# Optimization experiments

Hardware: AMD Instinct MI355X
Metric: run time of the kernel (lower is better)

## Reference

```python
import jax, jax.numpy as jnp
import numpy as np

B, C_IN, L = 4, 512, 16384
C_RED = C_IN // 2  # q/k/v reduced channels = 256
BL = 64            # sliding-window block size
NEG = -jnp.inf


def setup_inputs() -> dict:
    key = jax.random.key(0)
    ks = jax.random.split(key, 8)
    x1 = jax.random.normal(ks[0], (B, C_IN, L), dtype=jnp.float32)
    x2 = jax.random.normal(ks[1], (B, C_IN, L), dtype=jnp.float32)
    mask = jnp.ones((B, 1, L), dtype=jnp.float32)
    s = 0.02
    Wq = jax.random.normal(ks[2], (C_RED, C_IN), dtype=jnp.float32) * s
    Wk = jax.random.normal(ks[3], (C_RED, C_IN), dtype=jnp.float32) * s
    Wv = jax.random.normal(ks[4], (C_RED, C_IN), dtype=jnp.float32) * s
    Wo = jax.random.normal(ks[5], (C_IN, C_RED), dtype=jnp.float32) * s
    bq = jnp.zeros((C_RED,), jnp.float32)
    bk = jnp.zeros((C_RED,), jnp.float32)
    bv = jnp.zeros((C_RED,), jnp.float32)
    bo = jnp.zeros((C_IN,), jnp.float32)
    return {"x1": x1, "x2": x2, "mask": mask, "Wq": Wq, "bq": bq,
            "Wk": Wk, "bk": bk, "Wv": Wv, "bv": bv, "Wo": Wo, "bo": bo}


def _conv1x1(W, b, x):
    # x: (B, Cin, L) -> (B, Cout, L)
    return jnp.einsum('oc,bcl->bol', W, x) + b[None, :, None]


def reference(x1, x2, mask, Wq, bq, Wk, bk, Wv, bv, Wo, bo):
    # encoder stage: value comes from x1 (x2 unused)
    q = _conv1x1(Wq, bq, x1)  # (B, C, L)
    k = _conv1x1(Wk, bk, x1)
    v = _conv1x1(Wv, bv, x1)

    Bq, C, Lq = q.shape
    bl = BL
    nb = (Lq + bl - 1) // bl
    pad = nb * bl - Lq
    if pad > 0:
        q = jnp.pad(q, ((0, 0), (0, 0), (0, pad)))
        k = jnp.pad(k, ((0, 0), (0, 0), (0, pad)))
        v = jnp.pad(v, ((0, 0), (0, 0), (0, pad)))
        mask = jnp.pad(mask, ((0, 0), (0, 0), (0, pad)))

    # non-overlapping windows: (B, C, nb, bl)
    qb = q.reshape(Bq, C, nb, bl)
    kb = k.reshape(Bq, C, nb, bl)
    vb = v.reshape(Bq, C, nb, bl)
    mb = mask.reshape(Bq, 1, nb, bl)  # (B,1,nb,bl)

    scale = 1.0 / jnp.sqrt(jnp.float32(C))
    # per-block attention scores: (B, nb, bl_i, bl_j)
    scores = jnp.einsum('bcni,bcnj->bnij', qb, kb) * scale
    key_mask = mb[:, 0, :, None, :]  # (B, nb, 1, bl_j)
    scores = jnp.where(key_mask == 0, NEG, scores)
    probs = jax.nn.softmax(scores, axis=-1)
    attn = jnp.einsum('bnij,bcnj->bcni', probs, vb)  # (B, C, nb, bl)

    h = jax.nn.relu(attn)
    out = jnp.einsum('oc,bcni->boni', Wo, h) + bo[None, :, None, None]
    out = out.reshape(Bq, Wo.shape[0], nb * bl)
    if pad > 0:
        out = out[:, :, :Lq]
    return out
```

## Files before the change

### kernel.cpp

```cpp
#include <hip/hip_runtime.h>
#include <hip/hip_fp16.h>
#include <stdint.h>

#define BB    4
#define CIN   512
#define CRED  256
#define LL    16384
#define NBLK  256
#define WELEM 131072

typedef _Float16 half8 __attribute__((ext_vector_type(8)));
typedef float    f32x4 __attribute__((ext_vector_type(4)));

#define SWZ(r) (((r)&7)<<4)

#define QBASE   524288
#define MAT_E   16777216
#define WS_NEED ((size_t)(QBASE + 3 * MAT_E) * 2)

__global__ void convert_weights(const float* __restrict__ Wq,
                                const float* __restrict__ Wk,
                                const float* __restrict__ Wv,
                                const float* __restrict__ Wo,
                                _Float16* __restrict__ dst) {
    int i = blockIdx.x * blockDim.x + threadIdx.x;
    int m = i >> 17;
    int e = i & (WELEM - 1);
    const float* src = (m == 0) ? Wq : (m == 1) ? Wk : (m == 2) ? Wv : Wo;
    dst[(size_t)m * WELEM + e] = (_Float16)src[e];
}

__global__ __launch_bounds__(256, 2)
void qkv_gemm(const float* __restrict__ x1, const _Float16* __restrict__ W,
              const float* __restrict__ bq, const float* __restrict__ bk,
              const float* __restrict__ bv, _Float16* __restrict__ ws) {
    extern __shared__ char lds[];
    const int tid = threadIdx.x;
    const int wid = tid >> 6;
    const int l15 = tid & 15;
    const int l4  = (tid & 63) >> 4;
    const int b   = blockIdx.x >> 8;
    const int n   = blockIdx.x & 255;

    {
        const int jx = tid & 15;
        const int rg = tid >> 4;
        const float* xp = x1 + ((size_t)b * CIN + 8 * rg) * LL + n * 64 + 4 * jx;
        f32x4 st[4][8];
        #pragma unroll
        for (int i = 0; i < 4; ++i)
            #pragma unroll
            for (int r8 = 0; r8 < 8; ++r8)
                st[i][r8] = *(const f32x4*)(xp + (size_t)(128 * i + r8) * LL);
        asm volatile("" ::: "memory");
        #pragma unroll
        for (int i = 0; i < 4; ++i) {
            #pragma unroll
            for (int u = 0; u < 4; ++u) {
                const int j = 4 * jx + u;
                union { _Float16 h[8]; half8 v; } pk;
                #pragma unroll
                for (int r8 = 0; r8 < 8; ++r8) pk.h[r8] = (_Float16)st[i][r8][u];
                *(half8*)(lds + j * 1024 + ((16 * rg + 256 * i) ^ SWZ(j))) = pk.v;
            }
        }
    }
    __syncthreads();

    #pragma unroll
    for (int p = 0; p < 3; ++p) {
        f32x4 acc[4][4];
        #pragma unroll
        for (int mt = 0; mt < 4; ++mt)
            #pragma unroll
            for (int q = 0; q < 4; ++q) acc[mt][q] = (f32x4){0.f, 0.f, 0.f, 0.f};

        const _Float16* wp = W + (size_t)p * WELEM
                           + (size_t)(wid * 64 + l15) * CIN + l4 * 8;

        half8 wf[2][4], xf[2][4];
        #pragma unroll
        for (int mt = 0; mt < 4; ++mt) wf[0][mt] = *(const half8*)(wp + mt * 16 * CIN);
        #pragma unroll
        for (int nt = 0; nt < 4; ++nt) {
            const int j = nt * 16 + l15;
            xf[0][nt] = *(const half8*)(lds + j * 1024 + ((l4 * 16) ^ SWZ(j)));
        }

        #pragma unroll
        for (int ks = 0; ks < 16; ++ks) {
            const int c = ks & 1, nx = c ^ 1;
            if (ks < 15) {
                const int kb = (ks + 1) * 64 + l4 * 16;
                #pragma unroll
                for (int mt = 0; mt < 4; ++mt)
                    wf[nx][mt] = *(const half8*)(wp + mt * 16 * CIN + (ks + 1) * 32);
                #pragma unroll
                for (int nt = 0; nt < 4; ++nt) {
                    const int j = nt * 16 + l15;
                    xf[nx][nt] = *(const half8*)(lds + j * 1024 + (kb ^ SWZ(j)));
                }
            }
            #pragma unroll
            for (int mt = 0; mt < 4; ++mt)
                #pragma unroll
                for (int nt = 0; nt < 4; ++nt)
                    acc[mt][nt] = __builtin_amdgcn_mfma_f32_16x16x32_f16(
                        wf[c][mt], xf[c][nt], acc[mt][nt], 0, 0, 0);
        }

        if (p < 2) {
            _Float16* dst = ws + QBASE + (size_t)p * MAT_E
                          + ((size_t)b * LL + n * 64) * CRED;
            const float* bias = p ? bk : bq;
            #pragma unroll
            for (int mt = 0; mt < 4; ++mt) {
                const int c0 = wid * 64 + mt * 16 + l4 * 4;
                f32x4 b4 = *(const f32x4*)(bias + c0);
                #pragma unroll
                for (int nt = 0; nt < 4; ++nt) {
                    const int pos = nt * 16 + l15;
                    union { _Float16 h[4]; uint64_t q; } pk;
                    #pragma unroll
                    for (int ri = 0; ri < 4; ++ri)
                        pk.h[ri] = (_Float16)(acc[mt][nt][ri] + b4[ri]);
                    *(uint64_t*)(dst + (size_t)pos * CRED + c0) = pk.q;
                }
            }
        } else {
            _Float16* vdst = ws + QBASE + 2 * (size_t)MAT_E
                           + (size_t)b * CRED * LL + n * 64;
            #pragma unroll
            for (int mt = 0; mt < 4; ++mt) {
                const int c0 = wid * 64 + mt * 16 + l4 * 4;
                f32x4 b4 = *(const f32x4*)(bv + c0);
                #pragma unroll
                for (int nt = 0; nt < 4; ++nt) {
                    const int pos = nt * 16 + l15;
                    #pragma unroll
                    for (int ri = 0; ri < 4; ++ri)
                        vdst[(size_t)(c0 + ri) * LL + pos] =
                            (_Float16)(acc[mt][nt][ri] + b4[ri]);
                }
            }
        }
    }
}

#define BH_OFF 0
#define BP_OFF 32768
#define LDS_B  40960

__global__ __launch_bounds__(256, 3)
void attn_out(const float* __restrict__ mask, const _Float16* __restrict__ ws,
              const float* __restrict__ bo, float* __restrict__ out) {
    extern __shared__ char lds[];
    const int tid = threadIdx.x;
    const int wid = tid >> 6;
    const int l15 = tid & 15;
    const int l4  = (tid & 63) >> 4;
    const int b   = blockIdx.x >> 8;
    const int n   = blockIdx.x & 255;

    const _Float16* qt = ws + QBASE + ((size_t)b * LL + n * 64) * CRED;
    const _Float16* kt = qt + MAT_E;
    const _Float16* vt = ws + QBASE + 2 * (size_t)MAT_E + (size_t)b * CRED * LL + n * 64;
    const _Float16* Wo = ws + 3 * (size_t)WELEM;

    {
        const int i0 = wid * 16;
        f32x4 sa[4];
        #pragma unroll
        for (int jt = 0; jt < 4; ++jt) sa[jt] = (f32x4){0.f, 0.f, 0.f, 0.f};
        #pragma unroll
        for (int ks = 0; ks < 8; ++ks) {
            half8 qa = *(const half8*)(qt + (size_t)(i0 + l15) * CRED + ks * 32 + l4 * 8);
            #pragma unroll
            for (int jt = 0; jt < 4; ++jt) {
                half8 kf = *(const half8*)(kt + (size_t)(jt * 16 + l15) * CRED + ks * 32 + l4 * 8);
                sa[jt] = __builtin_amdgcn_mfma_f32_16x16x32_f16(qa, kf, sa[jt], 0, 0, 0);
            }
        }
        float msk[4];
        #pragma unroll
        for (int jt = 0; jt < 4; ++jt)
            msk[jt] = mask[(size_t)b * LL + n * 64 + jt * 16 + l15];
        #pragma unroll
        for (int ri = 0; ri < 4; ++ri) {
            float v[4];
            #pragma unroll
            for (int jt = 0; jt < 4; ++jt)
                v[jt] = (msk[jt] == 0.f) ? -1e30f : sa[jt][ri] * 0.0625f;
            float mx = fmaxf(fmaxf(v[0], v[1]), fmaxf(v[2], v[3]));
            mx = fmaxf(mx, __shfl_xor(mx, 1));
            mx = fmaxf(mx, __shfl_xor(mx, 2));
            mx = fmaxf(mx, __shfl_xor(mx, 4));
            mx = fmaxf(mx, __shfl_xor(mx, 8));
            float e[4], sum = 0.f;
            #pragma unroll
            for (int jt = 0; jt < 4; ++jt) { e[jt] = __expf(v[jt] - mx); sum += e[jt]; }
            sum += __shfl_xor(sum, 1);
            sum += __shfl_xor(sum, 2);
            sum += __shfl_xor(sum, 4);
            sum += __shfl_xor(sum, 8);
            const float inv = 1.f / sum;
            const int i = i0 + l4 * 4 + ri;
            #pragma unroll
            for (int jt = 0; jt < 4; ++jt) {
                const int j = jt * 16 + l15;
                *(_Float16*)(lds + BP_OFF + i * 128 + ((2 * j) ^ SWZ(i))) =
                    (_Float16)(e[jt] * inv);
            }
        }
    }
    __syncthreads();

    {
        const int cb = wid * 64;
        f32x4 pv[4][4];
        #pragma unroll
        for (int m = 0; m < 4; ++m)
            #pragma unroll
            for (int q = 0; q < 4; ++q) pv[m][q] = (f32x4){0.f, 0.f, 0.f, 0.f};
        #pragma unroll
        for (int ks = 0; ks < 2; ++ks) {
            const int kb = ks * 64 + l4 * 16;
            half8 pb[4];
            #pragma unroll
            for (int nt = 0; nt < 4; ++nt) {
                const int i = nt * 16 + l15;
                pb[nt] = *(const half8*)(lds + BP_OFF + i * 128 + (kb ^ SWZ(i)));
            }
            #pragma unroll
            for (int mt = 0; mt < 4; ++mt) {
                half8 va = *(const half8*)(vt + (size_t)(cb + mt * 16 + l15) * LL + ks * 32 + l4 * 8);
                #pragma unroll
                for (int nt = 0; nt < 4; ++nt)
                    pv[mt][nt] = __builtin_amdgcn_mfma_f32_16x16x32_f16(va, pb[nt], pv[mt][nt], 0, 0, 0);
            }
        }
        #pragma unroll
        for (int mt = 0; mt < 4; ++mt) {
            const int c0 = cb + mt * 16 + l4 * 4;
            #pragma unroll
            for (int nt = 0; nt < 4; ++nt) {
                const int j = nt * 16 + l15;
                union { _Float16 h[4]; uint64_t q; } hp;
                #pragma unroll
                for (int ri = 0; ri < 4; ++ri)
                    hp.h[ri] = (_Float16)fmaxf(pv[mt][nt][ri], 0.f);
                *(uint64_t*)(lds + BH_OFF + j * 512 + ((2 * c0) ^ SWZ(j))) = hp.q;
            }
        }
    }
    __syncthreads();

    #pragma unroll
    for (int op = 0; op < 2; ++op) {
        const int mbo = wid * 128 + op * 64;
        const _Float16* wob = Wo + (size_t)(mbo + l15) * CRED + l4 * 8;
        f32x4 oa[4][4];
        #pragma unroll
        for (int m = 0; m < 4; ++m)
            #pragma unroll
            for (int q = 0; q < 4; ++q) oa[m][q] = (f32x4){0.f, 0.f, 0.f, 0.f};
        #pragma unroll 4
        for (int ks = 0; ks < 8; ++ks) {
            const int kb = ks * 64 + l4 * 16;
            half8 hb[4];
            #pragma unroll
            for (int nt = 0; nt < 4; ++nt) {
                const int i = nt * 16 + l15;
                hb[nt] = *(const half8*)(lds + BH_OFF + i * 512 + (kb ^ SWZ(i)));
            }
            #pragma unroll
            for (int mt = 0; mt < 4; ++mt) {
                half8 wa = *(const half8*)(wob + mt * 16 * CRED + ks * 32);
                #pragma unroll
                for (int nt = 0; nt < 4; ++nt)
                    oa[mt][nt] = __builtin_amdgcn_mfma_f32_16x16x32_f16(wa, hb[nt], oa[mt][nt], 0, 0, 0);
            }
        }
        #pragma unroll
        for (int mt = 0; mt < 4; ++mt) {
            const int o0 = mbo + mt * 16 + l4 * 4;
            f32x4 bov = *(const f32x4*)(bo + o0);
            #pragma unroll
            for (int ri = 0; ri < 4; ++ri) {
                float* orow = out + ((size_t)b * CIN + (o0 + ri)) * LL + n * 64;
                #pragma unroll
                for (int nt = 0; nt < 4; ++nt)
                    orow[nt * 16 + l15] = oa[mt][nt][ri] + bov[ri];
            }
        }
    }
}

#define XT_OFF 0
#define Q_OFF  0
#define K_OFF  32768
#define V_OFF  32768
#define H_OFF  0
#define P_OFF  65536
#define MSK_OFF 73728
#define LDS_BYTES 73984

__global__ __launch_bounds__(256, 2)
void att_fused(const float* __restrict__ x1, const float* __restrict__ mask,
               const _Float16* __restrict__ W,
               const float* __restrict__ bq, const float* __restrict__ bk,
               const float* __restrict__ bv, const float* __restrict__ bo,
               float* __restrict__ out) {
    extern __shared__ char lds[];
    const int tid  = threadIdx.x;
    const int wid  = tid >> 6;
    const int lane = tid & 63;
    const int l15  = lane & 15;
    const int l4   = lane >> 4;
    const int blk  = blockIdx.x;
    const int b    = blk >> 8;
    const int n    = blk & 255;

    const _Float16* Wq = W;
    const _Float16* Wk = W + WELEM;
    const _Float16* Wv = W + 2 * WELEM;
    const _Float16* Wo = W + 3 * WELEM;

    {
        const int jx = tid & 15;
        const int rb = tid >> 4;
        const float* xbase = x1 + ((size_t)b * CIN + 2 * rb) * LL + n * 64 + 4 * jx;
        #pragma unroll
        for (int i = 0; i < 16; ++i) {
            f32x4 a = *(const f32x4*)(xbase + (size_t)(32 * i) * LL);
            f32x4 c = *(const f32x4*)(xbase + (size_t)(32 * i + 1) * LL);
            const int col = 4 * rb + 64 * i;
            #pragma unroll
            for (int u = 0; u < 4; ++u) {
                union { _Float16 h[2]; uint32_t w; } p;
                p.h[0] = (_Float16)a[u];
                p.h[1] = (_Float16)c[u];
                const int j = 4 * jx + u;
                *(uint32_t*)(lds + XT_OFF + j * 1024 + (col ^ SWZ(j))) = p.w;
            }
        }
        if (tid < 64)
            *(float*)(lds + MSK_OFF + tid * 4) = mask[(size_t)b * LL + n * 64 + tid];
    }
    __syncthreads();

    uint64_t qh[4][4], kh[4][4], vh[4][4];
    #pragma unroll
    for (int pass = 0; pass < 4; ++pass) {
        f32x4 aQ[4], aK[4], aV[4];
        #pragma unroll
        for (int q = 0; q < 4; ++q) {
            aQ[q] = (f32x4){0.f, 0.f, 0.f, 0.f};
            aK[q] = (f32x4){0.f, 0.f, 0.f, 0.f};
            aV[q] = (f32x4){0.f, 0.f, 0.f, 0.f};
        }
// ... 138 lines not shown
            }
            #pragma unroll
            for (int mt = 0; mt < 4; ++mt) {
                const int c = cb + mt * 16 + l15;
                half8 va = *(const half8*)(lds + V_OFF + c * 128 + (kb ^ SWZ(c)));
                #pragma unroll
                for (int nt = 0; nt < 4; ++nt)
                    pv[mt][nt] = __builtin_amdgcn_mfma_f32_16x16x32_f16(va, pb[nt], pv[mt][nt], 0, 0, 0);
            }
        }
        #pragma unroll
        for (int mt = 0; mt < 4; ++mt) {
            const int c0 = cb + mt * 16 + l4 * 4;
            #pragma unroll
            for (int nt = 0; nt < 4; ++nt) {
                const int j = nt * 16 + l15;
                union { _Float16 h[4]; uint64_t q; } hp;
                #pragma unroll
                for (int ri = 0; ri < 4; ++ri)
                    hp.h[ri] = (_Float16)fmaxf(pv[mt][nt][ri], 0.f);
                *(uint64_t*)(lds + H_OFF + j * 512 + ((2 * c0) ^ SWZ(j))) = hp.q;
            }
        }
    }
    __syncthreads();

    #pragma unroll
    for (int op = 0; op < 2; ++op) {
        const int mbo = wid * 128 + op * 64;
        const _Float16* wob = Wo + (size_t)(mbo + l15) * CRED + l4 * 8;
        f32x4 oa[4][4];
        #pragma unroll
        for (int m = 0; m < 4; ++m)
            #pragma unroll
            for (int q = 0; q < 4; ++q) oa[m][q] = (f32x4){0.f, 0.f, 0.f, 0.f};
        #pragma unroll 4
        for (int ks = 0; ks < 8; ++ks) {
            const int kb = ks * 64 + l4 * 16;
            half8 hb[4];
            #pragma unroll
            for (int nt = 0; nt < 4; ++nt) {
                const int i = nt * 16 + l15;
                hb[nt] = *(const half8*)(lds + H_OFF + i * 512 + (kb ^ SWZ(i)));
            }
            #pragma unroll
            for (int mt = 0; mt < 4; ++mt) {
                half8 wa = *(const half8*)(wob + mt * 16 * CRED + ks * 32);
                #pragma unroll
                for (int nt = 0; nt < 4; ++nt)
                    oa[mt][nt] = __builtin_amdgcn_mfma_f32_16x16x32_f16(wa, hb[nt], oa[mt][nt], 0, 0, 0);
            }
        }
        #pragma unroll
        for (int mt = 0; mt < 4; ++mt) {
            const int o0 = mbo + mt * 16 + l4 * 4;
            f32x4 bov = *(const f32x4*)(bo + o0);
            #pragma unroll
            for (int ri = 0; ri < 4; ++ri) {
                float* orow = out + ((size_t)b * CIN + (o0 + ri)) * LL + n * 64;
                #pragma unroll
                for (int nt = 0; nt < 4; ++nt)
                    orow[nt * 16 + l15] = oa[mt][nt][ri] + bov[ri];
            }
        }
    }
}

extern "C" void kernel_launch(void* const* d_in, const int* in_sizes, int n_in,
                              void* d_out, int out_size, void* d_ws, size_t ws_size,
                              hipStream_t stream) {
    const float* x1   = (const float*)d_in[0];
    const float* mask = (const float*)d_in[2];
    const float* Wq   = (const float*)d_in[3];
    const float* bq   = (const float*)d_in[4];
    const float* Wk   = (const float*)d_in[5];
    const float* bk   = (const float*)d_in[6];
    const float* Wv   = (const float*)d_in[7];
    const float* bv   = (const float*)d_in[8];
    const float* Wo   = (const float*)d_in[9];
    const float* bo   = (const float*)d_in[10];
    float* out = (float*)d_out;
    _Float16* wbuf = (_Float16*)d_ws;

    convert_weights<<<2048, 256, 0, stream>>>(Wq, Wk, Wv, Wo, wbuf);

    if (ws_size >= WS_NEED) {
        (void)hipFuncSetAttribute((const void*)qkv_gemm,
                                  hipFuncAttributeMaxDynamicSharedMemorySize, 65536);
        qkv_gemm<<<BB * NBLK, 256, 65536, stream>>>(x1, wbuf, bq, bk, bv, wbuf);
        attn_out<<<BB * NBLK, 256, LDS_B, stream>>>(mask, wbuf, bo, out);
    } else {
        (void)hipFuncSetAttribute((const void*)att_fused,
                                  hipFuncAttributeMaxDynamicSharedMemorySize, LDS_BYTES);
        att_fused<<<BB * NBLK, 256, LDS_BYTES, stream>>>(x1, mask, wbuf, bq, bk, bv, bo, out);
    }
}
```

Before: 199.0 us.

## Split x transpose into separate kernel and tile-local V layout in QKV GEMM

Adds an x_transpose kernel that converts x1 to fp16 and writes per-tile transposed blocks to workspace, so the QKV GEMM reads x fragments straight from global memory instead of staging them through 64KB of LDS. The GEMM now uses 512 threads with two m-tiles per wave. V is written into the x tile region it just consumed, stored contiguously as channel x 64 per tile rather than strided by L. This adds an extra kernel launch and a full fp16 round trip of x through memory, in exchange for higher occupancy and better-coalesced V stores and loads.

```diff
diff --git a/kernel.cpp b/kernel.cpp
--- a/kernel.cpp
+++ b/kernel.cpp
@@ -14,9 +14,12 @@
 
 #define SWZ(r) (((r)&7)<<4)
 
-#define QBASE   524288
-#define MAT_E   16777216
-#define WS_NEED ((size_t)(QBASE + 3 * MAT_E) * 2)
+#define XB      524288
+#define TILE_EL 32768
+#define XTV_EL  (1024 * TILE_EL)
+#define QB2     (XB + XTV_EL)
+#define KB2     (QB2 + 16777216)
+#define WS_NEED ((size_t)(KB2 + 16777216) * 2)
 
 __global__ void convert_weights(const float* __restrict__ Wq,
                                 const float* __restrict__ Wk,
@@ -30,79 +33,86 @@
     dst[(size_t)m * WELEM + e] = (_Float16)src[e];
 }
 
-__global__ __launch_bounds__(256, 2)
-void qkv_gemm(const float* __restrict__ x1, const _Float16* __restrict__ W,
-              const float* __restrict__ bq, const float* __restrict__ bk,
-              const float* __restrict__ bv, _Float16* __restrict__ ws) {
-    extern __shared__ char lds[];
+__global__ __launch_bounds__(256, 4)
+void x_transpose(const float* __restrict__ x1, _Float16* __restrict__ ws) {
+    __shared__ char lds[16384];
+    const int tid = threadIdx.x;
+    const int blk = blockIdx.x;
+    const int t   = blk >> 2;
+    const int cc  = blk & 3;
+    const int b   = t >> 8, n = t & 255;
+    const int jx  = tid & 15;
+    const int rg  = tid >> 4;
+
+    const float* xp = x1 + ((size_t)b * CIN + cc * 128 + 8 * rg) * LL + n * 64 + 4 * jx;
+    f32x4 r[8];
+    #pragma unroll
+    for (int k = 0; k < 8; ++k)
+        r[k] = *(const f32x4*)(xp + (size_t)k * LL);
+    asm volatile("" ::: "memory");
+    #pragma unroll
+    for (int u = 0; u < 4; ++u) {
+        const int j = 4 * jx + u;
+        union { _Float16 h[8]; half8 v; } pk;
+        #pragma unroll
+        for (int k = 0; k < 8; ++k) pk.h[k] = (_Float16)r[k][u];
+        *(half8*)(lds + j * 256 + ((16 * rg) ^ SWZ(j))) = pk.v;
+    }
+    __syncthreads();
+    _Float16* dst = ws + XB + (size_t)t * TILE_EL + cc * 8192;
+    const int l4d = tid >> 6, jd = tid & 63;
+    #pragma unroll
+    for (int rr = 0; rr < 4; ++rr) {
+        half8 v = *(const half8*)(lds + jd * 256 + ((rr * 64 + l4d * 16) ^ SWZ(jd)));
+        *(half8*)(dst + rr * 2048 + tid * 8) = v;
+    }
+}
+
+__global__ __launch_bounds__(512, 4)
+void qkv_gemm2(const _Float16* __restrict__ W,
+               const float* __restrict__ bq, const float* __restrict__ bk,
+               const float* __restrict__ bv, _Float16* ws) {
     const int tid = threadIdx.x;
     const int wid = tid >> 6;
     const int l15 = tid & 15;
     const int l4  = (tid & 63) >> 4;
-    const int b   = blockIdx.x >> 8;
-    const int n   = blockIdx.x & 255;
-
-    {
-        const int jx = tid & 15;
-        const int rg = tid >> 4;
-        const float* xp = x1 + ((size_t)b * CIN + 8 * rg) * LL + n * 64 + 4 * jx;
-        f32x4 st[4][8];
-        #pragma unroll
-        for (int i = 0; i < 4; ++i)
-            #pragma unroll
-            for (int r8 = 0; r8 < 8; ++r8)
-                st[i][r8] = *(const f32x4*)(xp + (size_t)(128 * i + r8) * LL);
-        asm volatile("" ::: "memory");
-        #pragma unroll
-        for (int i = 0; i < 4; ++i) {
-            #pragma unroll
-            for (int u = 0; u < 4; ++u) {
-                const int j = 4 * jx + u;
-                union { _Float16 h[8]; half8 v; } pk;
-                #pragma unroll
-                for (int r8 = 0; r8 < 8; ++r8) pk.h[r8] = (_Float16)st[i][r8][u];
-                *(half8*)(lds + j * 1024 + ((16 * rg + 256 * i) ^ SWZ(j))) = pk.v;
-            }
-        }
-    }
-    __syncthreads();
+    const int t   = blockIdx.x;
+    const int b   = t >> 8, n = t & 255;
+
+    const _Float16* xt = ws + XB + (size_t)t * TILE_EL;
+    f32x4 accV[2][4];
 
     #pragma unroll
     for (int p = 0; p < 3; ++p) {
-        f32x4 acc[4][4];
-        #pragma unroll
-        for (int mt = 0; mt < 4; ++mt)
+        f32x4 acc[2][4];
+        #pragma unroll
+        for (int mt = 0; mt < 2; ++mt)
             #pragma unroll
             for (int q = 0; q < 4; ++q) acc[mt][q] = (f32x4){0.f, 0.f, 0.f, 0.f};
 
         const _Float16* wp = W + (size_t)p * WELEM
-                           + (size_t)(wid * 64 + l15) * CIN + l4 * 8;
-
-        half8 wf[2][4], xf[2][4];
-        #pragma unroll
-        for (int mt = 0; mt < 4; ++mt) wf[0][mt] = *(const half8*)(wp + mt * 16 * CIN);
-        #pragma unroll
-        for (int nt = 0; nt < 4; ++nt) {
-            const int j = nt * 16 + l15;
-            xf[0][nt] = *(const half8*)(lds + j * 1024 + ((l4 * 16) ^ SWZ(j)));
-        }
+                           + (size_t)(wid * 32 + l15) * CIN + l4 * 8;
+        half8 wf[2][2], xf[2][4];
+        #pragma unroll
+        for (int mt = 0; mt < 2; ++mt) wf[0][mt] = *(const half8*)(wp + mt * 16 * CIN);
+        #pragma unroll
+        for (int nt = 0; nt < 4; ++nt)
+            xf[0][nt] = *(const half8*)(xt + l4 * 512 + (nt * 16 + l15) * 8);
 
         #pragma unroll
         for (int ks = 0; ks < 16; ++ks) {
             const int c = ks & 1, nx = c ^ 1;
             if (ks < 15) {
-                const int kb = (ks + 1) * 64 + l4 * 16;
-                #pragma unroll
-                for (int mt = 0; mt < 4; ++mt)
+                #pragma unroll
+                for (int mt = 0; mt < 2; ++mt)
                     wf[nx][mt] = *(const half8*)(wp + mt * 16 * CIN + (ks + 1) * 32);
                 #pragma unroll
-                for (int nt = 0; nt < 4; ++nt) {
-                    const int j = nt * 16 + l15;
-                    xf[nx][nt] = *(const half8*)(lds + j * 1024 + (kb ^ SWZ(j)));
-                }
-            }
-            #pragma unroll
-            for (int mt = 0; mt < 4; ++mt)
+                for (int nt = 0; nt < 4; ++nt)
+                    xf[nx][nt] = *(const half8*)(xt + (ks + 1) * 2048 + l4 * 512
+                                                 + (nt * 16 + l15) * 8);
+            }
+            #pragma unroll
+            for (int mt = 0; mt < 2; ++mt)
                 #pragma unroll
                 for (int nt = 0; nt < 4; ++nt)
                     acc[mt][nt] = __builtin_amdgcn_mfma_f32_16x16x32_f16(
@@ -110,12 +120,11 @@
         }
 
         if (p < 2) {
-            _Float16* dst = ws + QBASE + (size_t)p * MAT_E
-                          + ((size_t)b * LL + n * 64) * CRED;
+            _Float16* dst = ws + (p ? KB2 : QB2) + ((size_t)b * LL + n * 64) * CRED;
             const float* bias = p ? bk : bq;
             #pragma unroll
-            for (int mt = 0; mt < 4; ++mt) {
-                const int c0 = wid * 64 + mt * 16 + l4 * 4;
+            for (int mt = 0; mt < 2; ++mt) {
+                const int c0 = wid * 32 + mt * 16 + l4 * 4;
                 f32x4 b4 = *(const f32x4*)(bias + c0);
                 #pragma unroll
                 for (int nt = 0; nt < 4; ++nt) {
@@ -128,20 +137,27 @@
                 }
             }
         } else {
-            _Float16* vdst = ws + QBASE + 2 * (size_t)MAT_E
-                           + (size_t)b * CRED * LL + n * 64;
-            #pragma unroll
-            for (int mt = 0; mt < 4; ++mt) {
-                const int c0 = wid * 64 + mt * 16 + l4 * 4;
-                f32x4 b4 = *(const f32x4*)(bv + c0);
-                #pragma unroll
-                for (int nt = 0; nt < 4; ++nt) {
-                    const int pos = nt * 16 + l15;
-                    #pragma unroll
-                    for (int ri = 0; ri < 4; ++ri)
-                        vdst[(size_t)(c0 + ri) * LL + pos] =
-                            (_Float16)(acc[mt][nt][ri] + b4[ri]);
-                }
+            #pragma unroll
+            for (int mt = 0; mt < 2; ++mt)
+                #pragma unroll
+                for (int q = 0; q < 4; ++q) accV[mt][q] = acc[mt][q];
+        }
+    }
+
+    __syncthreads();
+    {
+        _Float16* vdst = ws + XB + (size_t)t * TILE_EL;
+        #pragma unroll
+        for (int mt = 0; mt < 2; ++mt) {
+            const int c0 = wid * 32 + mt * 16 + l4 * 4;
+            f32x4 b4 = *(const f32x4*)(bv + c0);
+            #pragma unroll
+            for (int nt = 0; nt < 4; ++nt) {
+                const int pos = nt * 16 + l15;
+                #pragma unroll
+                for (int ri = 0; ri < 4; ++ri)
+                    vdst[(size_t)(c0 + ri) * 64 + pos] =
+                        (_Float16)(accV[mt][nt][ri] + b4[ri]);
             }
         }
     }
@@ -161,10 +177,11 @@
     const int l4  = (tid & 63) >> 4;
     const int b   = blockIdx.x >> 8;
     const int n   = blockIdx.x & 255;
-
-    const _Float16* qt = ws + QBASE + ((size_t)b * LL + n * 64) * CRED;
-    const _Float16* kt = qt + MAT_E;
-    const _Float16* vt = ws + QBASE + 2 * (size_t)MAT_E + (size_t)b * CRED * LL + n * 64;
+    const int t   = blockIdx.x;
+
+    const _Float16* qt = ws + QB2 + ((size_t)b * LL + n * 64) * CRED;
+    const _Float16* kt = ws + KB2 + ((size_t)b * LL + n * 64) * CRED;
+    const _Float16* vt = ws + XB + (size_t)t * TILE_EL;
     const _Float16* Wo = ws + 3 * (size_t)WELEM;
 
     {
@@ -233,7 +250,7 @@
             }
             #pragma unroll
             for (int mt = 0; mt < 4; ++mt) {
-                half8 va = *(const half8*)(vt + (size_t)(cb + mt * 16 + l15) * LL + ks * 32 + l4 * 8);
+                half8 va = *(const half8*)(vt + (size_t)(cb + mt * 16 + l15) * 64 + ks * 32 + l4 * 8);
                 #pragma unroll
                 for (int nt = 0; nt < 4; ++nt)
                     pv[mt][nt] = __builtin_amdgcn_mfma_f32_16x16x32_f16(va, pb[nt], pv[mt][nt], 0, 0, 0);
@@ -583,9 +600,8 @@
     convert_weights<<<2048, 256, 0, stream>>>(Wq, Wk, Wv, Wo, wbuf);
 
     if (ws_size >= WS_NEED) {
-        (void)hipFuncSetAttribute((const void*)qkv_gemm,
-                                  hipFuncAttributeMaxDynamicSharedMemorySize, 65536);
-        qkv_gemm<<<BB * NBLK, 256, 65536, stream>>>(x1, wbuf, bq, bk, bv, wbuf);
+        x_transpose<<<4096, 256, 0, stream>>>(x1, wbuf);
+        qkv_gemm2<<<BB * NBLK, 512, 0, stream>>>(wbuf, bq, bk, bv, wbuf);
         attn_out<<<BB * NBLK, 256, LDS_B, stream>>>(mask, wbuf, bo, out);
     } else {
         (void)hipFuncSetAttribute((const void*)att_fused,
```

After: 261.2 us. 31.2% more time.

## Pre-swizzle weights into MFMA fragment layout and store V per-block contiguously

Applied to the files above, without the earlier changes.

Weights are converted into a fragment-major fp16 layout so each lane's half8 MFMA operand comes from a contiguous chunk, which makes weight loads coalesced. The QKV kernel now computes Q and K together in one pass over the LDS x tile, with staggered k-order per wave. V is staged through LDS and written as a contiguous per-block tile instead of strided rows of length L. The attention kernel reads V and Wo with the new layouts. The price is higher register pressure from the two live accumulator sets and the loss of the explicit double-buffered prefetch.

```diff
diff --git a/kernel.cpp b/kernel.cpp
--- a/kernel.cpp
+++ b/kernel.cpp
@@ -14,15 +14,38 @@
 
 #define SWZ(r) (((r)&7)<<4)
 
-#define QBASE   524288
-#define MAT_E   16777216
-#define WS_NEED ((size_t)(QBASE + 3 * MAT_E) * 2)
-
-__global__ void convert_weights(const float* __restrict__ Wq,
-                                const float* __restrict__ Wk,
-                                const float* __restrict__ Wv,
-                                const float* __restrict__ Wo,
-                                _Float16* __restrict__ dst) {
+#define QB      524288
+#define KB      (QB + 16777216)
+#define VB      (KB + 16777216)
+#define WS_NEED ((size_t)(VB + 16777216) * 2)
+
+__global__ void convert_weights_fm(const float* __restrict__ Wq,
+                                   const float* __restrict__ Wk,
+                                   const float* __restrict__ Wv,
+                                   const float* __restrict__ Wo,
+                                   _Float16* __restrict__ dst) {
+    int i = blockIdx.x * blockDim.x + threadIdx.x;
+    int p = i >> 17;
+    int e17 = i & (WELEM - 1);
+    const float* src = (p == 0) ? Wq : (p == 1) ? Wk : (p == 2) ? Wv : Wo;
+    const int Kd = (p < 3) ? 512 : 256;
+    const int sh = (p < 3) ? 13 : 12;
+    const int m16 = e17 >> sh;
+    const int rem = e17 & ((1 << sh) - 1);
+    const int ks  = rem >> 9;
+    const int l4  = (rem >> 7) & 3;
+    const int l15 = (rem >> 3) & 15;
+    const int ee  = rem & 7;
+    const int r = m16 * 16 + l15;
+    const int k = ks * 32 + l4 * 8 + ee;
+    dst[(size_t)p * WELEM + e17] = (_Float16)src[(size_t)r * Kd + k];
+}
+
+__global__ void convert_weights_rm(const float* __restrict__ Wq,
+                                   const float* __restrict__ Wk,
+                                   const float* __restrict__ Wv,
+                                   const float* __restrict__ Wo,
+                                   _Float16* __restrict__ dst) {
     int i = blockIdx.x * blockDim.x + threadIdx.x;
     int m = i >> 17;
     int e = i & (WELEM - 1);
@@ -31,16 +54,16 @@
 }
 
 __global__ __launch_bounds__(256, 2)
-void qkv_gemm(const float* __restrict__ x1, const _Float16* __restrict__ W,
-              const float* __restrict__ bq, const float* __restrict__ bk,
-              const float* __restrict__ bv, _Float16* __restrict__ ws) {
+void qkv_fused(const float* __restrict__ x1, const _Float16* __restrict__ W,
+               const float* __restrict__ bq, const float* __restrict__ bk,
+               const float* __restrict__ bv, _Float16* __restrict__ ws) {
     extern __shared__ char lds[];
     const int tid = threadIdx.x;
     const int wid = tid >> 6;
     const int l15 = tid & 15;
     const int l4  = (tid & 63) >> 4;
-    const int b   = blockIdx.x >> 8;
-    const int n   = blockIdx.x & 255;
+    const int t   = blockIdx.x;
+    const int b   = t >> 8, n = t & 255;
 
     {
         const int jx = tid & 15;
@@ -67,82 +90,113 @@
     }
     __syncthreads();
 
+    const int fbase = l4 * 128 + l15 * 8;
+
+    f32x4 aQ[4][4], aK[4][4];
     #pragma unroll
-    for (int p = 0; p < 3; ++p) {
-        f32x4 acc[4][4];
-        #pragma unroll
-        for (int mt = 0; mt < 4; ++mt)
-            #pragma unroll
-            for (int q = 0; q < 4; ++q) acc[mt][q] = (f32x4){0.f, 0.f, 0.f, 0.f};
-
-        const _Float16* wp = W + (size_t)p * WELEM
-                           + (size_t)(wid * 64 + l15) * CIN + l4 * 8;
-
-        half8 wf[2][4], xf[2][4];
-        #pragma unroll
-        for (int mt = 0; mt < 4; ++mt) wf[0][mt] = *(const half8*)(wp + mt * 16 * CIN);
-        #pragma unroll
-        for (int nt = 0; nt < 4; ++nt) {
-            const int j = nt * 16 + l15;
-            xf[0][nt] = *(const half8*)(lds + j * 1024 + ((l4 * 16) ^ SWZ(j)));
-        }
-
-        #pragma unroll
-        for (int ks = 0; ks < 16; ++ks) {
-            const int c = ks & 1, nx = c ^ 1;
-            if (ks < 15) {
-                const int kb = (ks + 1) * 64 + l4 * 16;
-                #pragma unroll
-                for (int mt = 0; mt < 4; ++mt)
-                    wf[nx][mt] = *(const half8*)(wp + mt * 16 * CIN + (ks + 1) * 32);
+    for (int mt = 0; mt < 4; ++mt)
+        #pragma unroll
+        for (int q = 0; q < 4; ++q) {
+            aQ[mt][q] = (f32x4){0.f, 0.f, 0.f, 0.f};
+            aK[mt][q] = (f32x4){0.f, 0.f, 0.f, 0.f};
+        }
+    {
+        const _Float16* wqf = W + (size_t)(wid * 4) * 8192 + fbase;
+        const _Float16* wkf = wqf + WELEM;
+        #pragma unroll
+        for (int i = 0; i < 16; ++i) {
+            const int ks = (i + wid * 4) & 15;
+            half8 xf[4];
+            #pragma unroll
+            for (int nt = 0; nt < 4; ++nt) {
+                const int j = nt * 16 + l15;
+                xf[nt] = *(const half8*)(lds + j * 1024 + ((ks * 64 + l4 * 16) ^ SWZ(j)));
+            }
+            #pragma unroll
+            for (int mt = 0; mt < 4; ++mt) {
+                half8 qf = *(const half8*)(wqf + mt * 8192 + ks * 512);
+                half8 kf = *(const half8*)(wkf + mt * 8192 + ks * 512);
                 #pragma unroll
                 for (int nt = 0; nt < 4; ++nt) {
-                    const int j = nt * 16 + l15;
-                    xf[nx][nt] = *(const half8*)(lds + j * 1024 + (kb ^ SWZ(j)));
+                    aQ[mt][nt] = __builtin_amdgcn_mfma_f32_16x16x32_f16(qf, xf[nt], aQ[mt][nt], 0, 0, 0);
+                    aK[mt][nt] = __builtin_amdgcn_mfma_f32_16x16x32_f16(kf, xf[nt], aK[mt][nt], 0, 0, 0);
                 }
             }
-            #pragma unroll
-            for (int mt = 0; mt < 4; ++mt)
+        }
+    }
+    {
+        _Float16* qdst = ws + QB + (size_t)t * 16384;
+        _Float16* kdst = ws + KB + (size_t)t * 16384;
+        #pragma unroll
+        for (int mt = 0; mt < 4; ++mt) {
+            const int c0 = wid * 64 + mt * 16 + l4 * 4;
+            f32x4 bq4 = *(const f32x4*)(bq + c0);
+            f32x4 bk4 = *(const f32x4*)(bk + c0);
+            #pragma unroll
+            for (int nt = 0; nt < 4; ++nt) {
+                const int pos = nt * 16 + l15;
+                union { _Float16 h[4]; uint64_t q; } qp, kp;
+                #pragma unroll
+                for (int ri = 0; ri < 4; ++ri) {
+                    qp.h[ri] = (_Float16)(aQ[mt][nt][ri] + bq4[ri]);
+                    kp.h[ri] = (_Float16)(aK[mt][nt][ri] + bk4[ri]);
+                }
+                *(uint64_t*)(qdst + (size_t)pos * 256 + c0) = qp.q;
+                *(uint64_t*)(kdst + (size_t)pos * 256 + c0) = kp.q;
+            }
+        }
+    }
+
+    f32x4 aV[4][4];
+    #pragma unroll
+    for (int mt = 0; mt < 4; ++mt)
+        #pragma unroll
+        for (int q = 0; q < 4; ++q) aV[mt][q] = (f32x4){0.f, 0.f, 0.f, 0.f};
+    {
+        const _Float16* wvf = W + 2 * (size_t)WELEM + (size_t)(wid * 4) * 8192 + fbase;
+        #pragma unroll
+        for (int i = 0; i < 16; ++i) {
+            const int ks = (i + wid * 4) & 15;
+            half8 xf[4];
+            #pragma unroll
+            for (int nt = 0; nt < 4; ++nt) {
+                const int j = nt * 16 + l15;
+                xf[nt] = *(const half8*)(lds + j * 1024 + ((ks * 64 + l4 * 16) ^ SWZ(j)));
+            }
+            #pragma unroll
+            for (int mt = 0; mt < 4; ++mt) {
+                half8 vf = *(const half8*)(wvf + mt * 8192 + ks * 512);
                 #pragma unroll
                 for (int nt = 0; nt < 4; ++nt)
-                    acc[mt][nt] = __builtin_amdgcn_mfma_f32_16x16x32_f16(
-                        wf[c][mt], xf[c][nt], acc[mt][nt], 0, 0, 0);
-        }
-
-        if (p < 2) {
-            _Float16* dst = ws + QBASE + (size_t)p * MAT_E
-                          + ((size_t)b * LL + n * 64) * CRED;
-            const float* bias = p ? bk : bq;
-            #pragma unroll
-            for (int mt = 0; mt < 4; ++mt) {
-                const int c0 = wid * 64 + mt * 16 + l4 * 4;
-                f32x4 b4 = *(const f32x4*)(bias + c0);
-                #pragma unroll
-                for (int nt = 0; nt < 4; ++nt) {
-                    const int pos = nt * 16 + l15;
-                    union { _Float16 h[4]; uint64_t q; } pk;
-                    #pragma unroll
-                    for (int ri = 0; ri < 4; ++ri)
-                        pk.h[ri] = (_Float16)(acc[mt][nt][ri] + b4[ri]);
-                    *(uint64_t*)(dst + (size_t)pos * CRED + c0) = pk.q;
-                }
-            }
-        } else {
-            _Float16* vdst = ws + QBASE + 2 * (size_t)MAT_E
-                           + (size_t)b * CRED * LL + n * 64;
-            #pragma unroll
-            for (int mt = 0; mt < 4; ++mt) {
-                const int c0 = wid * 64 + mt * 16 + l4 * 4;
-                f32x4 b4 = *(const f32x4*)(bv + c0);
-                #pragma unroll
-                for (int nt = 0; nt < 4; ++nt) {
-                    const int pos = nt * 16 + l15;
-                    #pragma unroll
-                    for (int ri = 0; ri < 4; ++ri)
-                        vdst[(size_t)(c0 + ri) * LL + pos] =
-                            (_Float16)(acc[mt][nt][ri] + b4[ri]);
-                }
-            }
+                    aV[mt][nt] = __builtin_amdgcn_mfma_f32_16x16x32_f16(vf, xf[nt], aV[mt][nt], 0, 0, 0);
+            }
+        }
+    }
+    __syncthreads();
+
+    {
+        _Float16* vl = (_Float16*)lds;
+        #pragma unroll
+        for (int mt = 0; mt < 4; ++mt) {
+            const int c0 = wid * 64 + mt * 16 + l4 * 4;
+            f32x4 bv4 = *(const f32x4*)(bv + c0);
+            #pragma unroll
+            for (int nt = 0; nt < 4; ++nt) {
+                const int pos = nt * 16 + l15;
+                #pragma unroll
+                for (int ri = 0; ri < 4; ++ri)
+                    vl[(size_t)(c0 + ri) * 64 + pos] = (_Float16)(aV[mt][nt][ri] + bv4[ri]);
+            }
+        }
+    }
+    __syncthreads();
+    {
+        _Float16* vdst = ws + VB + (size_t)t * 16384;
+        const _Float16* vl = (const _Float16*)lds;
+        #pragma unroll
+        for (int r = 0; r < 8; ++r) {
+            const int off = (r * 256 + tid) * 8;
+            *(half8*)(vdst + off) = *(const half8*)(vl + off);
         }
     }
 }
@@ -159,13 +213,13 @@
     const int wid = tid >> 6;
     const int l15 = tid & 15;
     const int l4  = (tid & 63) >> 4;
-    const int b   = blockIdx.x >> 8;
-    const int n   = blockIdx.x & 255;
-
-    const _Float16* qt = ws + QBASE + ((size_t)b * LL + n * 64) * CRED;
-    const _Float16* kt = qt + MAT_E;
-    const _Float16* vt = ws + QBASE + 2 * (size_t)MAT_E + (size_t)b * CRED * LL + n * 64;
-    const _Float16* Wo = ws + 3 * (size_t)WELEM;
+    const int t   = blockIdx.x;
+    const int b   = t >> 8, n = t & 255;
+
+    const _Float16* qt = ws + QB + (size_t)t * 16384;
+    const _Float16* kt = ws + KB + (size_t)t * 16384;
+    const _Float16* vt = ws + VB + (size_t)t * 16384;
+    const _Float16* WoF = ws + 3 * (size_t)WELEM;
 
     {
         const int i0 = wid * 16;
@@ -233,7 +287,7 @@
             }
             #pragma unroll
             for (int mt = 0; mt < 4; ++mt) {
-                half8 va = *(const half8*)(vt + (size_t)(cb + mt * 16 + l15) * LL + ks * 32 + l4 * 8);
+                half8 va = *(const half8*)(vt + (size_t)(cb + mt * 16 + l15) * 64 + ks * 32 + l4 * 8);
                 #pragma unroll
                 for (int nt = 0; nt < 4; ++nt)
                     pv[mt][nt] = __builtin_amdgcn_mfma_f32_16x16x32_f16(va, pb[nt], pv[mt][nt], 0, 0, 0);
@@ -258,12 +312,12 @@
     #pragma unroll
     for (int op = 0; op < 2; ++op) {
         const int mbo = wid * 128 + op * 64;
-        const _Float16* wob = Wo + (size_t)(mbo + l15) * CRED + l4 * 8;
         f32x4 oa[4][4];
         #pragma unroll
         for (int m = 0; m < 4; ++m)
             #pragma unroll
             for (int q = 0; q < 4; ++q) oa[m][q] = (f32x4){0.f, 0.f, 0.f, 0.f};
+        const _Float16* wof = WoF + (size_t)(wid * 8 + op * 4) * 4096 + l4 * 128 + l15 * 8;
         #pragma unroll 4
         for (int ks = 0; ks < 8; ++ks) {
             const int kb = ks * 64 + l4 * 16;
@@ -275,7 +329,7 @@
             }
             #pragma unroll
             for (int mt = 0; mt < 4; ++mt) {
-                half8 wa = *(const half8*)(wob + mt * 16 * CRED + ks * 32);
+                half8 wa = *(const half8*)(wof + mt * 4096 + ks * 512);
                 #pragma unroll
                 for (int nt = 0; nt < 4; ++nt)
                     oa[mt][nt] = __builtin_amdgcn_mfma_f32_16x16x32_f16(wa, hb[nt], oa[mt][nt], 0, 0, 0);
@@ -580,14 +634,14 @@
     float* out = (float*)d_out;
     _Float16* wbuf = (_Float16*)d_ws;
 
-    convert_weights<<<2048, 256, 0, stream>>>(Wq, Wk, Wv, Wo, wbuf);
-
     if (ws_size >= WS_NEED) {
-        (void)hipFuncSetAttribute((const void*)qkv_gemm,
+        convert_weights_fm<<<2048, 256, 0, stream>>>(Wq, Wk, Wv, Wo, wbuf);
+        (void)hipFuncSetAttribute((const void*)qkv_fused,
                                   hipFuncAttributeMaxDynamicSharedMemorySize, 65536);
-        qkv_gemm<<<BB * NBLK, 256, 65536, stream>>>(x1, wbuf, bq, bk, bv, wbuf);
+        qkv_fused<<<BB * NBLK, 256, 65536, stream>>>(x1, wbuf, bq, bk, bv, wbuf);
         attn_out<<<BB * NBLK, 256, LDS_B, stream>>>(mask, wbuf, bo, out);
     } else {
+        convert_weights_rm<<<2048, 256, 0, stream>>>(Wq, Wk, Wv, Wo, wbuf);
         (void)hipFuncSetAttribute((const void*)att_fused,
                                   hipFuncAttributeMaxDynamicSharedMemorySize, LDS_BYTES);
         att_fused<<<BB * NBLK, 256, LDS_BYTES, stream>>>(x1, mask, wbuf, bq, bk, bv, bo, out);
```

Measured after the change: 183.0 us. 8.1% less time.

## Split QKV projection across three grids with pipelined x staging and fragment-major weights

Applied to the files above, without the earlier changes.

The QKV GEMM now launches one block per (projection, batch, window), so grid size triples and each block computes a single projection. Each block streams x1 through a small double-buffered LDS tile, prefetching the next K-slice into registers while computing the current one. Weights are pre-permuted into MFMA fragment-major order so the per-lane weight loads are contiguous, and attn_out reads Wo in the same order. The cost is that every x1 tile is now read from global memory three times instead of once, traded for higher occupancy and less LDS per block.

```diff
diff --git a/kernel.cpp b/kernel.cpp
--- a/kernel.cpp
+++ b/kernel.cpp
@@ -14,15 +14,38 @@
 
 #define SWZ(r) (((r)&7)<<4)
 
-#define QBASE   524288
-#define MAT_E   16777216
-#define WS_NEED ((size_t)(QBASE + 3 * MAT_E) * 2)
-
-__global__ void convert_weights(const float* __restrict__ Wq,
-                                const float* __restrict__ Wk,
-                                const float* __restrict__ Wv,
-                                const float* __restrict__ Wo,
-                                _Float16* __restrict__ dst) {
+#define QB      524288
+#define KB      (QB + 16777216)
+#define VB      (KB + 16777216)
+#define WS_NEED ((size_t)(VB + 16777216) * 2)
+
+__global__ void convert_weights_fm(const float* __restrict__ Wq,
+                                   const float* __restrict__ Wk,
+                                   const float* __restrict__ Wv,
+                                   const float* __restrict__ Wo,
+                                   _Float16* __restrict__ dst) {
+    int i = blockIdx.x * blockDim.x + threadIdx.x;
+    int p = i >> 17;
+    int e17 = i & (WELEM - 1);
+    const float* src = (p == 0) ? Wq : (p == 1) ? Wk : (p == 2) ? Wv : Wo;
+    const int Kd = (p < 3) ? 512 : 256;
+    const int sh = (p < 3) ? 13 : 12;
+    const int m16 = e17 >> sh;
+    const int rem = e17 & ((1 << sh) - 1);
+    const int ks  = rem >> 9;
+    const int l4  = (rem >> 7) & 3;
+    const int l15 = (rem >> 3) & 15;
+    const int ee  = rem & 7;
+    const int r = m16 * 16 + l15;
+    const int k = ks * 32 + l4 * 8 + ee;
+    dst[(size_t)p * WELEM + e17] = (_Float16)src[(size_t)r * Kd + k];
+}
+
+__global__ void convert_weights_rm(const float* __restrict__ Wq,
+                                   const float* __restrict__ Wk,
+                                   const float* __restrict__ Wv,
+                                   const float* __restrict__ Wo,
+                                   _Float16* __restrict__ dst) {
     int i = blockIdx.x * blockDim.x + threadIdx.x;
     int m = i >> 17;
     int e = i & (WELEM - 1);
@@ -30,118 +53,112 @@
     dst[(size_t)m * WELEM + e] = (_Float16)src[e];
 }
 
-__global__ __launch_bounds__(256, 2)
-void qkv_gemm(const float* __restrict__ x1, const _Float16* __restrict__ W,
-              const float* __restrict__ bq, const float* __restrict__ bk,
-              const float* __restrict__ bv, _Float16* __restrict__ ws) {
-    extern __shared__ char lds[];
+__global__ __launch_bounds__(256, 3)
+void qkv_v4(const float* __restrict__ x1, const _Float16* __restrict__ W,
+            const float* __restrict__ bq, const float* __restrict__ bk,
+            const float* __restrict__ bv, _Float16* __restrict__ ws) {
+    __shared__ _Float16 bt[2][4096];
     const int tid = threadIdx.x;
     const int wid = tid >> 6;
     const int l15 = tid & 15;
     const int l4  = (tid & 63) >> 4;
-    const int b   = blockIdx.x >> 8;
-    const int n   = blockIdx.x & 255;
-
-    {
-        const int jx = tid & 15;
-        const int rg = tid >> 4;
-        const float* xp = x1 + ((size_t)b * CIN + 8 * rg) * LL + n * 64 + 4 * jx;
-        f32x4 st[4][8];
-        #pragma unroll
-        for (int i = 0; i < 4; ++i)
-            #pragma unroll
-            for (int r8 = 0; r8 < 8; ++r8)
-                st[i][r8] = *(const f32x4*)(xp + (size_t)(128 * i + r8) * LL);
-        asm volatile("" ::: "memory");
-        #pragma unroll
-        for (int i = 0; i < 4; ++i) {
-            #pragma unroll
-            for (int u = 0; u < 4; ++u) {
-                const int j = 4 * jx + u;
-                union { _Float16 h[8]; half8 v; } pk;
-                #pragma unroll
-                for (int r8 = 0; r8 < 8; ++r8) pk.h[r8] = (_Float16)st[i][r8][u];
-                *(half8*)(lds + j * 1024 + ((16 * rg + 256 * i) ^ SWZ(j))) = pk.v;
-            }
-        }
-    }
-    __syncthreads();
-
+    const int p   = blockIdx.x >> 10;
+    const int t   = blockIdx.x & 1023;
+    const int b   = t >> 8, n = t & 255;
+
+    const int c4 = tid & 15;
+    const int pq = tid >> 4;
+    const float* xb = x1 + ((size_t)b * CIN + 4 * c4) * LL + n * 64 + 4 * pq;
+    const int sH  = c4 >> 3;
+    const int l4b = (c4 >> 1) & 3;
+    const int e0  = (c4 & 1) * 4;
+
+    f32x4 st[4];
+    #define X_ISSUE(KT) do {                                                  \
+        _Pragma("unroll")                                                     \
+        for (int i_ = 0; i_ < 4; ++i_)                                        \
+            st[i_] = *(const f32x4*)(xb + (size_t)((KT) * 64 + i_) * LL);     \
+    } while (0)
+    #define X_COMMIT(BUF) do {                                                \
+        _Pragma("unroll")                                                     \
+        for (int u_ = 0; u_ < 4; ++u_) {                                      \
+            union { _Float16 h[4]; uint64_t q; } pk_;                         \
+            _Pragma("unroll")                                                 \
+            for (int i_ = 0; i_ < 4; ++i_) pk_.h[i_] = (_Float16)st[i_][u_];  \
+            *(uint64_t*)(&bt[BUF][sH * 2048 + l4b * 512 + (4 * pq + u_) * 8 + e0]) = pk_.q; \
+        }                                                                     \
+    } while (0)
+
+    X_ISSUE(0);
+    X_COMMIT(0);
+    __syncthreads();
+
+    f32x4 acc[4][4];
     #pragma unroll
-    for (int p = 0; p < 3; ++p) {
-        f32x4 acc[4][4];
-        #pragma unroll
-        for (int mt = 0; mt < 4; ++mt)
-            #pragma unroll
-            for (int q = 0; q < 4; ++q) acc[mt][q] = (f32x4){0.f, 0.f, 0.f, 0.f};
-
-        const _Float16* wp = W + (size_t)p * WELEM
-                           + (size_t)(wid * 64 + l15) * CIN + l4 * 8;
-
-        half8 wf[2][4], xf[2][4];
-        #pragma unroll
-        for (int mt = 0; mt < 4; ++mt) wf[0][mt] = *(const half8*)(wp + mt * 16 * CIN);
-        #pragma unroll
-        for (int nt = 0; nt < 4; ++nt) {
-            const int j = nt * 16 + l15;
-            xf[0][nt] = *(const half8*)(lds + j * 1024 + ((l4 * 16) ^ SWZ(j)));
-        }
-
-        #pragma unroll
-        for (int ks = 0; ks < 16; ++ks) {
-            const int c = ks & 1, nx = c ^ 1;
-            if (ks < 15) {
-                const int kb = (ks + 1) * 64 + l4 * 16;
-                #pragma unroll
-                for (int mt = 0; mt < 4; ++mt)
-                    wf[nx][mt] = *(const half8*)(wp + mt * 16 * CIN + (ks + 1) * 32);
-                #pragma unroll
-                for (int nt = 0; nt < 4; ++nt) {
-                    const int j = nt * 16 + l15;
-                    xf[nx][nt] = *(const half8*)(lds + j * 1024 + (kb ^ SWZ(j)));
-                }
-            }
+    for (int mt = 0; mt < 4; ++mt)
+        #pragma unroll
+        for (int q = 0; q < 4; ++q) acc[mt][q] = (f32x4){0.f, 0.f, 0.f, 0.f};
+
+    const _Float16* wf0 = W + (size_t)p * WELEM + (size_t)(wid * 4) * 8192
+                        + l4 * 128 + l15 * 8;
+
+    #pragma unroll
+    for (int kt = 0; kt < 8; ++kt) {
+        const int cur = kt & 1;
+        if (kt < 7) X_ISSUE(kt + 1);
+        #pragma unroll
+        for (int s = 0; s < 2; ++s) {
+            const int ks = kt * 2 + s;
+            half8 xf[4], wf[4];
+            #pragma unroll
+            for (int nt = 0; nt < 4; ++nt)
+                xf[nt] = *(const half8*)(&bt[cur][s * 2048 + l4 * 512 + (nt * 16 + l15) * 8]);
+            #pragma unroll
+            for (int mt = 0; mt < 4; ++mt)
+                wf[mt] = *(const half8*)(wf0 + mt * 8192 + ks * 512);
             #pragma unroll
             for (int mt = 0; mt < 4; ++mt)
                 #pragma unroll
                 for (int nt = 0; nt < 4; ++nt)
                     acc[mt][nt] = __builtin_amdgcn_mfma_f32_16x16x32_f16(
-                        wf[c][mt], xf[c][nt], acc[mt][nt], 0, 0, 0);
-        }
-
-        if (p < 2) {
-            _Float16* dst = ws + QBASE + (size_t)p * MAT_E
-                          + ((size_t)b * LL + n * 64) * CRED;
-            const float* bias = p ? bk : bq;
-            #pragma unroll
-            for (int mt = 0; mt < 4; ++mt) {
-                const int c0 = wid * 64 + mt * 16 + l4 * 4;
-                f32x4 b4 = *(const f32x4*)(bias + c0);
-                #pragma unroll
-                for (int nt = 0; nt < 4; ++nt) {
-                    const int pos = nt * 16 + l15;
-                    union { _Float16 h[4]; uint64_t q; } pk;
-                    #pragma unroll
-                    for (int ri = 0; ri < 4; ++ri)
-                        pk.h[ri] = (_Float16)(acc[mt][nt][ri] + b4[ri]);
-                    *(uint64_t*)(dst + (size_t)pos * CRED + c0) = pk.q;
-                }
-            }
-        } else {
-            _Float16* vdst = ws + QBASE + 2 * (size_t)MAT_E
-                           + (size_t)b * CRED * LL + n * 64;
-            #pragma unroll
-            for (int mt = 0; mt < 4; ++mt) {
-                const int c0 = wid * 64 + mt * 16 + l4 * 4;
-                f32x4 b4 = *(const f32x4*)(bv + c0);
-                #pragma unroll
-                for (int nt = 0; nt < 4; ++nt) {
-                    const int pos = nt * 16 + l15;
-                    #pragma unroll
-                    for (int ri = 0; ri < 4; ++ri)
-                        vdst[(size_t)(c0 + ri) * LL + pos] =
-                            (_Float16)(acc[mt][nt][ri] + b4[ri]);
-                }
+                        wf[mt], xf[nt], acc[mt][nt], 0, 0, 0);
+        }
+        if (kt < 7) X_COMMIT(cur ^ 1);
+        __syncthreads();
+    }
+    #undef X_ISSUE
+    #undef X_COMMIT
+
+    const float* bias = (p == 0) ? bq : (p == 1) ? bk : bv;
+    if (p < 2) {
+        _Float16* dst = ws + (p ? KB : QB) + ((size_t)b * LL + n * 64) * CRED;
+        #pragma unroll
+        for (int mt = 0; mt < 4; ++mt) {
+            const int c0 = wid * 64 + mt * 16 + l4 * 4;
+            f32x4 b4 = *(const f32x4*)(bias + c0);
+            #pragma unroll
+            for (int nt = 0; nt < 4; ++nt) {
+                const int pos = nt * 16 + l15;
+                union { _Float16 h[4]; uint64_t q; } pk;
+                #pragma unroll
+                for (int ri = 0; ri < 4; ++ri)
+                    pk.h[ri] = (_Float16)(acc[mt][nt][ri] + b4[ri]);
+                *(uint64_t*)(dst + (size_t)pos * CRED + c0) = pk.q;
+            }
+        }
+    } else {
+        _Float16* vd = ws + VB + (size_t)b * CRED * LL + n * 64;
+        #pragma unroll
+        for (int mt = 0; mt < 4; ++mt) {
+            const int c0 = wid * 64 + mt * 16 + l4 * 4;
+            f32x4 b4 = *(const f32x4*)(bias + c0);
+            #pragma unroll
+            for (int nt = 0; nt < 4; ++nt) {
+                const int pos = nt * 16 + l15;
+                #pragma unroll
+                for (int ri = 0; ri < 4; ++ri)
+                    vd[(size_t)(c0 + ri) * LL + pos] =
+                        (_Float16)(acc[mt][nt][ri] + b4[ri]);
             }
         }
     }
@@ -162,10 +179,10 @@
     const int b   = blockIdx.x >> 8;
     const int n   = blockIdx.x & 255;
 
-    const _Float16* qt = ws + QBASE + ((size_t)b * LL + n * 64) * CRED;
-    const _Float16* kt = qt + MAT_E;
-    const _Float16* vt = ws + QBASE + 2 * (size_t)MAT_E + (size_t)b * CRED * LL + n * 64;
-    const _Float16* Wo = ws + 3 * (size_t)WELEM;
+    const _Float16* qt = ws + QB + ((size_t)b * LL + n * 64) * CRED;
+    const _Float16* kt = ws + KB + ((size_t)b * LL + n * 64) * CRED;
+    const _Float16* vt = ws + VB + (size_t)b * CRED * LL + n * 64;
+    const _Float16* WoF = ws + 3 * (size_t)WELEM;
 
     {
         const int i0 = wid * 16;
@@ -258,12 +275,12 @@
     #pragma unroll
     for (int op = 0; op < 2; ++op) {
         const int mbo = wid * 128 + op * 64;
-        const _Float16* wob = Wo + (size_t)(mbo + l15) * CRED + l4 * 8;
         f32x4 oa[4][4];
         #pragma unroll
         for (int m = 0; m < 4; ++m)
             #pragma unroll
             for (int q = 0; q < 4; ++q) oa[m][q] = (f32x4){0.f, 0.f, 0.f, 0.f};
+        const _Float16* wof = WoF + (size_t)(wid * 8 + op * 4) * 4096 + l4 * 128 + l15 * 8;
         #pragma unroll 4
         for (int ks = 0; ks < 8; ++ks) {
             const int kb = ks * 64 + l4 * 16;
@@ -275,7 +292,7 @@
             }
             #pragma unroll
             for (int mt = 0; mt < 4; ++mt) {
-                half8 wa = *(const half8*)(wob + mt * 16 * CRED + ks * 32);
+                half8 wa = *(const half8*)(wof + mt * 4096 + ks * 512);
                 #pragma unroll
                 for (int nt = 0; nt < 4; ++nt)
                     oa[mt][nt] = __builtin_amdgcn_mfma_f32_16x16x32_f16(wa, hb[nt], oa[mt][nt], 0, 0, 0);
@@ -580,14 +597,12 @@
     float* out = (float*)d_out;
     _Float16* wbuf = (_Float16*)d_ws;
 
-    convert_weights<<<2048, 256, 0, stream>>>(Wq, Wk, Wv, Wo, wbuf);
-
     if (ws_size >= WS_NEED) {
-        (void)hipFuncSetAttribute((const void*)qkv_gemm,
-                                  hipFuncAttributeMaxDynamicSharedMemorySize, 65536);
-        qkv_gemm<<<BB * NBLK, 256, 65536, stream>>>(x1, wbuf, bq, bk, bv, wbuf);
+        convert_weights_fm<<<2048, 256, 0, stream>>>(Wq, Wk, Wv, Wo, wbuf);
+        qkv_v4<<<3 * BB * NBLK, 256, 0, stream>>>(x1, wbuf, bq, bk, bv, wbuf);
         attn_out<<<BB * NBLK, 256, LDS_B, stream>>>(mask, wbuf, bo, out);
     } else {
+        convert_weights_rm<<<2048, 256, 0, stream>>>(Wq, Wk, Wv, Wo, wbuf);
         (void)hipFuncSetAttribute((const void*)att_fused,
                                   hipFuncAttributeMaxDynamicSharedMemorySize, LDS_BYTES);
         att_fused<<<BB * NBLK, 256, LDS_BYTES, stream>>>(x1, mask, wbuf, bq, bk, bv, bo, out);
```

Measured after the change: 173.2 us. 13.0% less time.
